# Performance work log

Measured on AMD Instinct MI355X. Metric: run time of the kernel, lower is better.

The kernel has to match this reference:

```python
import jax, jax.numpy as jnp
import numpy as np

NHEAD = 8
HEAD_DIM = 32  # per-head dim d; C = NHEAD * HEAD_DIM = 256
NEG_INF = -1e9


def setup_inputs() -> dict:
    key = jax.random.key(0)
    k1, k2, k3, k4, k5 = jax.random.split(key, 5)
    B, L, C = 8, 1024, NHEAD * HEAD_DIM
    query = jax.random.normal(k1, (B, L, C), dtype=jnp.float32)
    key_t = jax.random.normal(k2, (B, L, C), dtype=jnp.float32)
    value = jax.random.normal(k3, (B, L, C), dtype=jnp.float32)
    hard_mask = jax.random.randint(k4, (B, L), 0, 2).astype(bool)
    bias = jax.random.normal(k5, (B, L, L), dtype=jnp.float32)
    return {"query": query, "key": key_t, "value": value,
            "hard_mask": hard_mask, "bias": bias}


def reference(query, key, value, hard_mask, bias):
    # Faithful to the hard-mask path: attention is computed only among
    # active tokens (hard_mask True); inactive positions pass `value` through.
    # Masking inactive KEYS with -inf in the softmax is mathematically
    # identical to the sort/gather/slice/SDPA/scatter-unsort in the original.
    B, L, C = query.shape
    H, D = NHEAD, HEAD_DIM
    scale = 1.0 / jnp.sqrt(jnp.asarray(D, query.dtype))

    def split_heads(t):  # (B, L, C) -> (B, H, L, D)
        return t.reshape(B, L, H, D).transpose(0, 2, 1, 3)

    q, k, v = split_heads(query), split_heads(key), split_heads(value)

    # scores: (B, H, Lq, Lk); bias broadcasts over heads
    scores = jnp.einsum('bhld,bhmd->bhlm', q, k) * scale + bias[:, None, :, :]
    scores = jnp.where(hard_mask[:, None, None, :], scores, NEG_INF)
    attn = jax.nn.softmax(scores, axis=-1)
    out = jnp.einsum('bhlm,bhmd->bhld', attn, v)          # (B, H, L, D)
    out = out.transpose(0, 2, 1, 3).reshape(B, L, C)      # (B, L, C)

    # inactive query positions return the raw value (scatter-back behavior)
    out = jnp.where(hard_mask[:, :, None], out, value)

    # torch.stack over per-item (1, L, C) results -> (B, 1, L, C)
    return out[:, None, :, :]
```

## Files before the change

### kernel.cpp

```cpp
#include <hip/hip_runtime.h>
#include <hip/hip_bf16.h>

#define B_    8
#define H_    8
#define L_    1024
#define D_    32
#define C_    256
#define NK    64
#define PSTR  72

typedef __attribute__((ext_vector_type(8))) short bf16x8;
typedef __attribute__((ext_vector_type(4))) float f32x4;

__device__ inline unsigned short f2bf(float f) {
    union { float f; unsigned int u; } x; x.f = f;
    return (unsigned short)((x.u + 0x7fffu + ((x.u >> 16) & 1u)) >> 16);
}

__device__ inline unsigned int pk_bf16(float lo, float hi) {
    union { __hip_bfloat162 h; unsigned int u; } c;
    c.h = __float22bfloat162_rn(make_float2(lo, hi));
    return c.u;
}

__global__ __launch_bounds__(256) void prep_kv(
    const float* __restrict__ k, const float* __restrict__ v,
    unsigned short* __restrict__ kbf, unsigned short* __restrict__ vt)
{
    const int tid = threadIdx.x;
    const int blk = blockIdx.x;
    __shared__ float sTf[32][65];

    if (blk < 1024) {
        const size_t g = (size_t)blk * 2048 + (size_t)tid * 8;
        const int b   = (int)(g >> 18);
        const int r1  = (int)(g & 262143);
        const int key = r1 >> 8;
        const int h   = (r1 >> 5) & 7;
        const int d0  = r1 & 31;
        float4 f0 = ((const float4*)(k + g))[0];
        float4 f1 = ((const float4*)(k + g))[1];
        uint4 o;
        o.x = pk_bf16(f0.x, f0.y);
        o.y = pk_bf16(f0.z, f0.w);
        o.z = pk_bf16(f1.x, f1.y);
        o.w = pk_bf16(f1.z, f1.w);
        *(uint4*)(kbf + ((size_t)((b * 8 + h) * 1024 + key) * 32 + d0)) = o;
    } else {
        const int bid = blk - 1024;
        const int bh = bid >> 4, c = bid & 15;
        const int b = bh >> 3, h = bh & 7;
        {
            const int row = tid >> 2, d8 = (tid & 3) * 8;
            const float* src = v + ((size_t)(b * L_ + c * 64 + row) * C_ + h * D_ + d8);
            float4 a = ((const float4*)src)[0];
            float4 cc = ((const float4*)src)[1];
            sTf[d8 + 0][row] = a.x;  sTf[d8 + 1][row] = a.y;
            sTf[d8 + 2][row] = a.z;  sTf[d8 + 3][row] = a.w;
            sTf[d8 + 4][row] = cc.x; sTf[d8 + 5][row] = cc.y;
            sTf[d8 + 6][row] = cc.z; sTf[d8 + 7][row] = cc.w;
        }
        __syncthreads();
        {
            const int d = tid >> 3, seg = tid & 7;
            uint4 o;
            o.x = pk_bf16(sTf[d][seg * 8 + 0], sTf[d][seg * 8 + 1]);
            o.y = pk_bf16(sTf[d][seg * 8 + 2], sTf[d][seg * 8 + 3]);
            o.z = pk_bf16(sTf[d][seg * 8 + 4], sTf[d][seg * 8 + 5]);
            o.w = pk_bf16(sTf[d][seg * 8 + 6], sTf[d][seg * 8 + 7]);
            const int ap = seg ^ (d & 7);
            *(uint4*)(vt + ((size_t)((bh * 16 + c) * 32 + d) * 64 + ap * 8)) = o;
        }
    }
}

__global__ __launch_bounds__(256, 4) void attn_main(
    const float* __restrict__ q,
    const float* __restrict__ v,
    const int*   __restrict__ mask,
    const float* __restrict__ bias,
    const unsigned short* __restrict__ kbf,
    const unsigned short* __restrict__ vt,
    float*       __restrict__ out)
{
    __shared__ __align__(16) unsigned short sK[2][NK * D_];
    __shared__ __align__(16) unsigned short sV[2][D_ * NK];
    __shared__ float sMadd[L_];
    __shared__ __align__(16) unsigned short sP[4][16][PSTR];

    const int tid  = threadIdx.x;
    const int wv   = tid >> 6;
    const int ln   = tid & 63;
    const int l16  = ln & 15;
    const int quad = ln >> 4;

    const int blk = blockIdx.x;
    const int h   = blk >> 7;
    const int rem = blk & 127;
    const int b   = rem >> 4;
    const int qt  = rem & 15;
    const int q0  = qt * 64 + wv * 16;
    const int bh  = b * H_ + h;

    const float scale = 0.17677669529663687f;

    {
        int4 m = ((const int4*)(mask + b * L_))[tid];
        sMadd[tid * 4 + 0] = m.x ? 0.f : -1e9f;
        sMadd[tid * 4 + 1] = m.y ? 0.f : -1e9f;
        sMadd[tid * 4 + 2] = m.z ? 0.f : -1e9f;
        sMadd[tid * 4 + 3] = m.w ? 0.f : -1e9f;
    }

    bf16x8 qfrag;
    {
        const float* qp = q + ((size_t)(b * L_ + q0 + l16) * C_ + h * D_ + quad * 8);
        float4 a = ((const float4*)qp)[0];
        float4 c = ((const float4*)qp)[1];
        __align__(16) unsigned int u[4] = {
            pk_bf16(a.x, a.y), pk_bf16(a.z, a.w),
            pk_bf16(c.x, c.y), pk_bf16(c.z, c.w)};
        qfrag = *(const bf16x8*)u;
    }

    const unsigned short* kt  = kbf + (size_t)bh * L_ * D_;
    const unsigned short* vtb = vt  + (size_t)bh * 16 * D_ * NK;

    uint4 kreg = *(const uint4*)(kt  + tid * 8);
    uint4 vreg = *(const uint4*)(vtb + tid * 8);
    *(uint4*)(&sK[0][tid * 8]) = kreg;
    *(uint4*)(&sV[0][tid * 8]) = vreg;
    __syncthreads();

    f32x4 Oacc[2] = {{0.f,0.f,0.f,0.f},{0.f,0.f,0.f,0.f}};
    float psum[4] = {0.f, 0.f, 0.f, 0.f};
    const size_t brow0 = (size_t)(b * L_ + q0 + quad * 4) * L_;

    for (int c = 0; c < 16; ++c) {
        const int cur = c & 1;
        const int j0  = c * NK;

        if (c < 15) {
            kreg = *(const uint4*)(kt  + (c + 1) * 2048 + tid * 8);
            vreg = *(const uint4*)(vtb + (c + 1) * 2048 + tid * 8);
        }

        float bz[4][4];
#pragma unroll
        for (int nt = 0; nt < 4; ++nt)
#pragma unroll
            for (int r = 0; r < 4; ++r)
                bz[nt][r] = bias[brow0 + (size_t)r * L_ + j0 + nt * 16 + l16];

        bf16x8 kf[4];
#pragma unroll
        for (int nt = 0; nt < 4; ++nt)
            kf[nt] = *(const bf16x8*)&sK[cur][(nt * 16 + l16) * D_ + quad * 8];

        f32x4 S[4];
#pragma unroll
        for (int nt = 0; nt < 4; ++nt)
            S[nt] = __builtin_amdgcn_mfma_f32_16x16x32_bf16(
                qfrag, kf[nt], (f32x4){0.f,0.f,0.f,0.f}, 0, 0, 0);

        float madd[4];
#pragma unroll
        for (int nt = 0; nt < 4; ++nt)
            madd[nt] = sMadd[j0 + nt * 16 + l16];

#pragma unroll
        for (int nt = 0; nt < 4; ++nt) {
#pragma unroll
            for (int r = 0; r < 4; ++r) {
                float t = bz[nt][r] + madd[nt];
                float p = __expf(fmaf(S[nt][r], scale, t));
                psum[r] += p;
                S[nt][r] = p;
            }
        }

#pragma unroll
        for (int nt = 0; nt < 4; ++nt) {
#pragma unroll
            for (int r = 0; r < 4; r += 2) {
                unsigned int u = pk_bf16(S[nt][r], S[nt][r + 1]);
                sP[wv][quad * 4 + r    ][nt * 16 + l16] = (unsigned short)u;
                sP[wv][quad * 4 + r + 1][nt * 16 + l16] = (unsigned short)(u >> 16);
            }
        }

#pragma unroll
        for (int s2 = 0; s2 < 2; ++s2) {
            bf16x8 pf = *(const bf16x8*)&sP[wv][l16][s2 * 32 + quad * 8];
#pragma unroll
            for (int nt = 0; nt < 2; ++nt) {
                const int d  = nt * 16 + l16;
                const int ap = (s2 * 4 + quad) ^ (l16 & 7);
                bf16x8 vf = *(const bf16x8*)&sV[cur][d * NK + ap * 8];
                Oacc[nt] = __builtin_amdgcn_mfma_f32_16x16x32_bf16(pf, vf, Oacc[nt], 0, 0, 0);
            }
        }

        if (c < 15) {
            *(uint4*)(&sK[cur ^ 1][tid * 8]) = kreg;
            *(uint4*)(&sV[cur ^ 1][tid * 8]) = vreg;
            __syncthreads();
        }
    }

#pragma unroll
    for (int r = 0; r < 4; ++r) {
        float t = psum[r];
        t += __shfl_xor(t, 1);
        t += __shfl_xor(t, 2);
        t += __shfl_xor(t, 4);
        t += __shfl_xor(t, 8);
        const int qrow = q0 + quad * 4 + r;
        const float inv = 1.f / t;
        const bool active = (sMadd[qrow] == 0.f);
        const size_t base = (size_t)(b * L_ + qrow) * C_ + h * D_;
#pragma unroll
        for (int nt = 0; nt < 2; ++nt) {
            const size_t idx = base + nt * 16 + l16;
            out[idx] = active ? Oacc[nt][r] * inv : v[idx];
        }
    }
}

#define MQ    64
#define KSTR  48
#define VSTR  72

__global__ __launch_bounds__(256) void masked_attn_mfma(
    const float* __restrict__ q,
    const float* __restrict__ k,
    const float* __restrict__ v,
    const int*   __restrict__ mask,
    const float* __restrict__ bias,
    float*       __restrict__ out)
{
    __shared__ __align__(16) unsigned short sQ[MQ][KSTR];
    __shared__ __align__(16) unsigned short sKt[NK][KSTR];
    __shared__ __align__(16) unsigned short sVt[D_][VSTR];
    __shared__ __align__(16) unsigned short sP2[4][16][VSTR];
    __shared__ float sMadd2[NK];

    const int tid  = threadIdx.x;
    const int wv   = tid >> 6;
    const int ln   = tid & 63;
    const int l16  = ln & 15;
    const int quad = ln >> 4;

    const int blk = blockIdx.x;
    const int h   = blk & 7;
    const int qt  = (blk >> 3) & 15;
    const int b   = blk >> 7;
    const int q0  = qt * MQ;
    const float scale = 0.17677669529663687f;

    {
        const int row = tid >> 2, d0 = (tid & 3) * 8;
        const float* src = q + ((size_t)(b * L_ + q0 + row) * C_ + h * D_ + d0);
        float4 a = ((const float4*)src)[0];
        float4 c = ((const float4*)src)[1];
        __align__(16) unsigned short t8[8] = {
            f2bf(a.x), f2bf(a.y), f2bf(a.z), f2bf(a.w),
            f2bf(c.x), f2bf(c.y), f2bf(c.z), f2bf(c.w)};
        *(int4*)&sQ[row][d0] = *(const int4*)t8;
    }
    __syncthreads();

    const bf16x8 qfrag = *(const bf16x8*)&sQ[wv * 16 + l16][quad * 8];
    f32x4 Oacc[2] = {{0.f,0.f,0.f,0.f},{0.f,0.f,0.f,0.f}};
    float lsum[4] = {0.f, 0.f, 0.f, 0.f};

    for (int j0 = 0; j0 < L_; j0 += NK) {
        __syncthreads();
        {
            const int row = tid >> 2, d0 = (tid & 3) * 8;
            const size_t src = (size_t)(b * L_ + j0 + row) * C_ + h * D_ + d0;
            float4 ka = ((const float4*)(k + src))[0];
            float4 kb = ((const float4*)(k + src))[1];
            __align__(16) unsigned short t8[8] = {
                f2bf(ka.x), f2bf(ka.y), f2bf(ka.z), f2bf(ka.w),
                f2bf(kb.x), f2bf(kb.y), f2bf(kb.z), f2bf(kb.w)};
            *(int4*)&sKt[row][d0] = *(const int4*)t8;

            float4 va = ((const float4*)(v + src))[0];
            float4 vb = ((const float4*)(v + src))[1];
            sVt[d0 + 0][row] = f2bf(va.x);
            sVt[d0 + 1][row] = f2bf(va.y);
            sVt[d0 + 2][row] = f2bf(va.z);
            sVt[d0 + 3][row] = f2bf(va.w);
            sVt[d0 + 4][row] = f2bf(vb.x);
            sVt[d0 + 5][row] = f2bf(vb.y);
            sVt[d0 + 6][row] = f2bf(vb.z);
            sVt[d0 + 7][row] = f2bf(vb.w);
            if (tid < NK) sMadd2[tid] = mask[b * L_ + j0 + tid] ? 0.f : -1e9f;
        }
        __syncthreads();

        bf16x8 kf[4];
#pragma unroll
        for (int nt = 0; nt < 4; ++nt)
            kf[nt] = *(const bf16x8*)&sKt[nt * 16 + l16][quad * 8];

        f32x4 S[4];
#pragma unroll
        for (int nt = 0; nt < 4; ++nt)
            S[nt] = __builtin_amdgcn_mfma_f32_16x16x32_bf16(
                qfrag, kf[nt], (f32x4){0.f,0.f,0.f,0.f}, 0, 0, 0);

        float psum[4] = {0.f, 0.f, 0.f, 0.f};
        const size_t brow0 = (size_t)(b * L_ + q0 + wv * 16 + quad * 4) * L_ + j0;
#pragma unroll
        for (int nt = 0; nt < 4; ++nt) {
            const float madd = sMadd2[nt * 16 + l16];
#pragma unroll
            for (int r = 0; r < 4; ++r) {
                float s = S[nt][r] * scale + bias[brow0 + (size_t)r * L_ + nt * 16 + l16] + madd;
                float p = __expf(s);
                psum[r] += p;
                S[nt][r] = p;
            }
        }
#pragma unroll
        for (int nt = 0; nt < 4; ++nt)
#pragma unroll
            for (int r = 0; r < 4; ++r)
                sP2[wv][quad * 4 + r][nt * 16 + l16] = f2bf(S[nt][r]);
#pragma unroll
        for (int r = 0; r < 4; ++r) {
            float t = psum[r];
            t += __shfl_xor(t, 1);
            t += __shfl_xor(t, 2);
            t += __shfl_xor(t, 4);
            t += __shfl_xor(t, 8);
            lsum[r] += t;
        }
#pragma unroll
        for (int s2 = 0; s2 < 2; ++s2) {
            bf16x8 pf = *(const bf16x8*)&sP2[wv][l16][s2 * 32 + quad * 8];
#pragma unroll
            for (int nt = 0; nt < 2; ++nt) {
                bf16x8 vf = *(const bf16x8*)&sVt[nt * 16 + l16][s2 * 32 + quad * 8];
                Oacc[nt] = __builtin_amdgcn_mfma_f32_16x16x32_bf16(pf, vf, Oacc[nt], 0, 0, 0);
            }
        }
    }
#pragma unroll
    for (int r = 0; r < 4; ++r) {
        const int qg = q0 + wv * 16 + quad * 4 + r;
        const int active = mask[b * L_ + qg];
        const size_t obase = (size_t)(b * L_ + qg) * C_ + h * D_;
        const float inv = 1.f / lsum[r];
#pragma unroll
        for (int nt = 0; nt < 2; ++nt) {
            float val;
            if (active) val = Oacc[nt][r] * inv;
            else        val = v[obase + nt * 16 + l16];
            out[obase + nt * 16 + l16] = val;
        }
    }
}

extern "C" void kernel_launch(void* const* d_in, const int* in_sizes, int n_in,
                              void* d_out, int out_size, void* d_ws, size_t ws_size,
                              hipStream_t stream) {
    const float* q    = (const float*)d_in[0];
    const float* k    = (const float*)d_in[1];
    const float* v    = (const float*)d_in[2];
    const int*   mask = (const int*)d_in[3];
    const float* bias = (const float*)d_in[4];
    float* out = (float*)d_out;

    if (ws_size >= (size_t)8 * 1024 * 1024) {
        unsigned short* kbf = (unsigned short*)d_ws;
        unsigned short* vt  = kbf + (size_t)2 * 1024 * 1024;
        prep_kv<<<2048, 256, 0, stream>>>(k, v, kbf, vt);
        attn_main<<<1024, 256, 0, stream>>>(q, v, mask, bias, kbf, vt, out);
    } else {
        masked_attn_mfma<<<1024, 256, 0, stream>>>(q, k, v, mask, bias, out);
    }
}
```

Baseline: 124.8 us.

## Pre-pack K/V into MFMA fragment layout and drop LDS staging in attention loop

The prep kernel now writes K and V as bf16 in the exact per-lane MFMA fragment order, so the main kernel loads fragments straight from global memory without shared-memory double buffering or per-chunk barriers. Scores pass through LDS in fp32, so bias is read row-contiguous as float4 and added together with the mask after the transpose. Scale is folded into Q, and the row sums are computed by an extra MFMA against a ones vector instead of a shuffle reduction. The cost is per-wave global fragment loads with no cross-wave reuse and no explicit prefetch, plus one more MFMA per sub-tile.

```diff
diff --git a/kernel.cpp b/kernel.cpp
--- a/kernel.cpp
+++ b/kernel.cpp
@@ -7,7 +7,6 @@
 #define D_    32
 #define C_    256
 #define NK    64
-#define PSTR  72
 
 typedef __attribute__((ext_vector_type(8))) short bf16x8;
 typedef __attribute__((ext_vector_type(4))) float f32x4;
@@ -23,70 +22,67 @@
     return c.u;
 }
 
-__global__ __launch_bounds__(256) void prep_kv(
+__global__ __launch_bounds__(256) void prep_frag(
     const float* __restrict__ k, const float* __restrict__ v,
-    unsigned short* __restrict__ kbf, unsigned short* __restrict__ vt)
+    unsigned short* __restrict__ kfrag, unsigned short* __restrict__ vfrag)
 {
     const int tid = threadIdx.x;
     const int blk = blockIdx.x;
-    __shared__ float sTf[32][65];
-
-    if (blk < 1024) {
-        const size_t g = (size_t)blk * 2048 + (size_t)tid * 8;
-        const int b   = (int)(g >> 18);
-        const int r1  = (int)(g & 262143);
-        const int key = r1 >> 8;
-        const int h   = (r1 >> 5) & 7;
-        const int d0  = r1 & 31;
-        float4 f0 = ((const float4*)(k + g))[0];
-        float4 f1 = ((const float4*)(k + g))[1];
-        uint4 o;
-        o.x = pk_bf16(f0.x, f0.y);
-        o.y = pk_bf16(f0.z, f0.w);
-        o.z = pk_bf16(f1.x, f1.y);
-        o.w = pk_bf16(f1.z, f1.w);
-        *(uint4*)(kbf + ((size_t)((b * 8 + h) * 1024 + key) * 32 + d0)) = o;
-    } else {
-        const int bid = blk - 1024;
-        const int bh = bid >> 4, c = bid & 15;
-        const int b = bh >> 3, h = bh & 7;
-        {
-            const int row = tid >> 2, d8 = (tid & 3) * 8;
-            const float* src = v + ((size_t)(b * L_ + c * 64 + row) * C_ + h * D_ + d8);
-            float4 a = ((const float4*)src)[0];
-            float4 cc = ((const float4*)src)[1];
-            sTf[d8 + 0][row] = a.x;  sTf[d8 + 1][row] = a.y;
-            sTf[d8 + 2][row] = a.z;  sTf[d8 + 3][row] = a.w;
-            sTf[d8 + 4][row] = cc.x; sTf[d8 + 5][row] = cc.y;
-            sTf[d8 + 6][row] = cc.z; sTf[d8 + 7][row] = cc.w;
-        }
-        __syncthreads();
-        {
-            const int d = tid >> 3, seg = tid & 7;
-            uint4 o;
-            o.x = pk_bf16(sTf[d][seg * 8 + 0], sTf[d][seg * 8 + 1]);
-            o.y = pk_bf16(sTf[d][seg * 8 + 2], sTf[d][seg * 8 + 3]);
-            o.z = pk_bf16(sTf[d][seg * 8 + 4], sTf[d][seg * 8 + 5]);
-            o.w = pk_bf16(sTf[d][seg * 8 + 6], sTf[d][seg * 8 + 7]);
-            const int ap = seg ^ (d & 7);
-            *(uint4*)(vt + ((size_t)((bh * 16 + c) * 32 + d) * 64 + ap * 8)) = o;
-        }
-    }
-}
-
-__global__ __launch_bounds__(256, 4) void attn_main(
+    const int bh = blk >> 4, c = blk & 15;
+    const int b = bh >> 3, h = bh & 7;
+
+    __shared__ float sKf[64 * 36];
+    __shared__ float sVf[64 * 33];
+
+    {
+        const int row = tid >> 2, seg = tid & 3;
+        const size_t src = (size_t)(b * L_ + c * 64 + row) * C_ + h * D_ + seg * 8;
+        float4 a = *(const float4*)(k + src);
+        float4 d = *(const float4*)(k + src + 4);
+        *(float4*)(sKf + row * 36 + seg * 8) = a;
+        *(float4*)(sKf + row * 36 + seg * 8 + 4) = d;
+        float4 va = *(const float4*)(v + src);
+        float4 vd = *(const float4*)(v + src + 4);
+        float* vr = sVf + row * 33 + seg * 8;
+        vr[0] = va.x; vr[1] = va.y; vr[2] = va.z; vr[3] = va.w;
+        vr[4] = vd.x; vr[5] = vd.y; vr[6] = vd.z; vr[7] = vd.w;
+    }
+    __syncthreads();
+
+    const int ln = tid & 63, u = tid >> 6;
+    const int l16 = ln & 15, quad = ln >> 4;
+
+    {
+        const float* src = sKf + (u * 16 + l16) * 36 + quad * 8;
+        float4 a = *(const float4*)src;
+        float4 d = *(const float4*)(src + 4);
+        uint4 o = { pk_bf16(a.x, a.y), pk_bf16(a.z, a.w),
+                    pk_bf16(d.x, d.y), pk_bf16(d.z, d.w) };
+        *(uint4*)(kfrag + (size_t)blk * 2048 + u * 512 + ln * 8) = o;
+    }
+    {
+        const int s2 = u >> 1, nt = u & 1;
+        float vals[8];
+#pragma unroll
+        for (int j = 0; j < 8; ++j)
+            vals[j] = sVf[(s2 * 32 + quad * 8 + j) * 33 + nt * 16 + l16];
+        uint4 o = { pk_bf16(vals[0], vals[1]), pk_bf16(vals[2], vals[3]),
+                    pk_bf16(vals[4], vals[5]), pk_bf16(vals[6], vals[7]) };
+        *(uint4*)(vfrag + (size_t)blk * 2048 + s2 * 1024 + nt * 512 + ln * 8) = o;
+    }
+}
+
+__global__ __launch_bounds__(256, 4) void attn_fa(
     const float* __restrict__ q,
     const float* __restrict__ v,
     const int*   __restrict__ mask,
     const float* __restrict__ bias,
-    const unsigned short* __restrict__ kbf,
-    const unsigned short* __restrict__ vt,
+    const unsigned short* __restrict__ kfrag,
+    const unsigned short* __restrict__ vfrag,
     float*       __restrict__ out)
 {
-    __shared__ __align__(16) unsigned short sK[2][NK * D_];
-    __shared__ __align__(16) unsigned short sV[2][D_ * NK];
     __shared__ float sMadd[L_];
-    __shared__ __align__(16) unsigned short sP[4][16][PSTR];
+    __shared__ float sS[4][16 * 68];
 
     const int tid  = threadIdx.x;
     const int wv   = tid >> 6;
@@ -111,6 +107,7 @@
         sMadd[tid * 4 + 2] = m.z ? 0.f : -1e9f;
         sMadd[tid * 4 + 3] = m.w ? 0.f : -1e9f;
     }
+    __syncthreads();
 
     bf16x8 qfrag;
     {
@@ -118,105 +115,87 @@
         float4 a = ((const float4*)qp)[0];
         float4 c = ((const float4*)qp)[1];
         __align__(16) unsigned int u[4] = {
-            pk_bf16(a.x, a.y), pk_bf16(a.z, a.w),
-            pk_bf16(c.x, c.y), pk_bf16(c.z, c.w)};
+            pk_bf16(a.x * scale, a.y * scale), pk_bf16(a.z * scale, a.w * scale),
+            pk_bf16(c.x * scale, c.y * scale), pk_bf16(c.z * scale, c.w * scale)};
         qfrag = *(const bf16x8*)u;
     }
 
-    const unsigned short* kt  = kbf + (size_t)bh * L_ * D_;
-    const unsigned short* vtb = vt  + (size_t)bh * 16 * D_ * NK;
-
-    uint4 kreg = *(const uint4*)(kt  + tid * 8);
-    uint4 vreg = *(const uint4*)(vtb + tid * 8);
-    *(uint4*)(&sK[0][tid * 8]) = kreg;
-    *(uint4*)(&sV[0][tid * 8]) = vreg;
-    __syncthreads();
+    bf16x8 onesf;
+#pragma unroll
+    for (int i = 0; i < 8; ++i) onesf[i] = (short)0x3F80;
+
+    const unsigned short* kf_base = kfrag + (size_t)bh * 32768 + ln * 8;
+    const unsigned short* vf_base = vfrag + (size_t)bh * 32768 + ln * 8;
+    const float* bias_row = bias + (size_t)(b * L_ + q0 + l16) * L_;
+    float* const sSw   = &sS[wv][0];
+    const float* sSrow = &sS[wv][0] + l16 * 68;
 
     f32x4 Oacc[2] = {{0.f,0.f,0.f,0.f},{0.f,0.f,0.f,0.f}};
-    float psum[4] = {0.f, 0.f, 0.f, 0.f};
-    const size_t brow0 = (size_t)(b * L_ + q0 + quad * 4) * L_;
+    f32x4 Lacc    = {0.f,0.f,0.f,0.f};
 
     for (int c = 0; c < 16; ++c) {
-        const int cur = c & 1;
-        const int j0  = c * NK;
-
-        if (c < 15) {
-            kreg = *(const uint4*)(kt  + (c + 1) * 2048 + tid * 8);
-            vreg = *(const uint4*)(vtb + (c + 1) * 2048 + tid * 8);
-        }
-
-        float bz[4][4];
+        const int j0 = c * NK;
+
+        const unsigned short* kp = kf_base + c * 2048;
+        bf16x8 kf0 = *(const bf16x8*)(kp);
+        bf16x8 kf1 = *(const bf16x8*)(kp + 512);
+        bf16x8 kf2 = *(const bf16x8*)(kp + 1024);
+        bf16x8 kf3 = *(const bf16x8*)(kp + 1536);
+
+        f32x4 S[4];
+        S[0] = __builtin_amdgcn_mfma_f32_16x16x32_bf16(qfrag, kf0, (f32x4){0.f,0.f,0.f,0.f}, 0, 0, 0);
+        S[1] = __builtin_amdgcn_mfma_f32_16x16x32_bf16(qfrag, kf1, (f32x4){0.f,0.f,0.f,0.f}, 0, 0, 0);
+        S[2] = __builtin_amdgcn_mfma_f32_16x16x32_bf16(qfrag, kf2, (f32x4){0.f,0.f,0.f,0.f}, 0, 0, 0);
+        S[3] = __builtin_amdgcn_mfma_f32_16x16x32_bf16(qfrag, kf3, (f32x4){0.f,0.f,0.f,0.f}, 0, 0, 0);
+
 #pragma unroll
         for (int nt = 0; nt < 4; ++nt)
 #pragma unroll
             for (int r = 0; r < 4; ++r)
-                bz[nt][r] = bias[brow0 + (size_t)r * L_ + j0 + nt * 16 + l16];
-
-        bf16x8 kf[4];
-#pragma unroll
-        for (int nt = 0; nt < 4; ++nt)
-            kf[nt] = *(const bf16x8*)&sK[cur][(nt * 16 + l16) * D_ + quad * 8];
-
-        f32x4 S[4];
-#pragma unroll
-        for (int nt = 0; nt < 4; ++nt)
-            S[nt] = __builtin_amdgcn_mfma_f32_16x16x32_bf16(
-                qfrag, kf[nt], (f32x4){0.f,0.f,0.f,0.f}, 0, 0, 0);
-
-        float madd[4];
-#pragma unroll
-        for (int nt = 0; nt < 4; ++nt)
-            madd[nt] = sMadd[j0 + nt * 16 + l16];
-
-#pragma unroll
-        for (int nt = 0; nt < 4; ++nt) {
-#pragma unroll
-            for (int r = 0; r < 4; ++r) {
-                float t = bz[nt][r] + madd[nt];
-                float p = __expf(fmaf(S[nt][r], scale, t));
-                psum[r] += p;
-                S[nt][r] = p;
+                sSw[(quad * 4 + r) * 68 + nt * 16 + l16] = S[nt][r];
+
+        bf16x8 pf[2];
+#pragma unroll
+        for (int s2 = 0; s2 < 2; ++s2) {
+            const float* sr = sSrow + s2 * 32 + quad * 8;
+            float4 a0 = *(const float4*)(sr);
+            float4 a1 = *(const float4*)(sr + 4);
+            const float* bp = bias_row + j0 + s2 * 32 + quad * 8;
+            float4 b0 = *(const float4*)(bp);
+            float4 b1 = *(const float4*)(bp + 4);
+            const float* mp = sMadd + j0 + s2 * 32 + quad * 8;
+            float4 m0 = *(const float4*)(mp);
+            float4 m1 = *(const float4*)(mp + 4);
+            float p0 = __expf(a0.x + b0.x + m0.x);
+            float p1 = __expf(a0.y + b0.y + m0.y);
+            float p2 = __expf(a0.z + b0.z + m0.z);
+            float p3 = __expf(a0.w + b0.w + m0.w);
+            float p4 = __expf(a1.x + b1.x + m1.x);
+            float p5 = __expf(a1.y + b1.y + m1.y);
+            float p6 = __expf(a1.z + b1.z + m1.z);
+            float p7 = __expf(a1.w + b1.w + m1.w);
+            __align__(16) unsigned int u[4] = {
+                pk_bf16(p0, p1), pk_bf16(p2, p3),
+                pk_bf16(p4, p5), pk_bf16(p6, p7)};
+            pf[s2] = *(const bf16x8*)u;
+        }
+
+        const unsigned short* vp = vf_base + c * 2048;
+#pragma unroll
+        for (int s2 = 0; s2 < 2; ++s2) {
+            Lacc = __builtin_amdgcn_mfma_f32_16x16x32_bf16(pf[s2], onesf, Lacc, 0, 0, 0);
+#pragma unroll
+            for (int nt = 0; nt < 2; ++nt) {
+                bf16x8 vfr = *(const bf16x8*)(vp + s2 * 1024 + nt * 512);
+                Oacc[nt] = __builtin_amdgcn_mfma_f32_16x16x32_bf16(pf[s2], vfr, Oacc[nt], 0, 0, 0);
             }
         }
-
-#pragma unroll
-        for (int nt = 0; nt < 4; ++nt) {
-#pragma unroll
-            for (int r = 0; r < 4; r += 2) {
-                unsigned int u = pk_bf16(S[nt][r], S[nt][r + 1]);
-                sP[wv][quad * 4 + r    ][nt * 16 + l16] = (unsigned short)u;
-                sP[wv][quad * 4 + r + 1][nt * 16 + l16] = (unsigned short)(u >> 16);
-            }
-        }
-
-#pragma unroll
-        for (int s2 = 0; s2 < 2; ++s2) {
-            bf16x8 pf = *(const bf16x8*)&sP[wv][l16][s2 * 32 + quad * 8];
-#pragma unroll
-            for (int nt = 0; nt < 2; ++nt) {
-                const int d  = nt * 16 + l16;
-                const int ap = (s2 * 4 + quad) ^ (l16 & 7);
-                bf16x8 vf = *(const bf16x8*)&sV[cur][d * NK + ap * 8];
-                Oacc[nt] = __builtin_amdgcn_mfma_f32_16x16x32_bf16(pf, vf, Oacc[nt], 0, 0, 0);
-            }
-        }
-
-        if (c < 15) {
-            *(uint4*)(&sK[cur ^ 1][tid * 8]) = kreg;
-            *(uint4*)(&sV[cur ^ 1][tid * 8]) = vreg;
-            __syncthreads();
-        }
     }
 
 #pragma unroll
     for (int r = 0; r < 4; ++r) {
-        float t = psum[r];
-        t += __shfl_xor(t, 1);
-        t += __shfl_xor(t, 2);
-        t += __shfl_xor(t, 4);
-        t += __shfl_xor(t, 8);
         const int qrow = q0 + quad * 4 + r;
-        const float inv = 1.f / t;
+        const float inv = 1.f / Lacc[r];
         const bool active = (sMadd[qrow] == 0.f);
         const size_t base = (size_t)(b * L_ + qrow) * C_ + h * D_;
 #pragma unroll
@@ -375,10 +354,10 @@
     float* out = (float*)d_out;
 
     if (ws_size >= (size_t)8 * 1024 * 1024) {
-        unsigned short* kbf = (unsigned short*)d_ws;
-        unsigned short* vt  = kbf + (size_t)2 * 1024 * 1024;
-        prep_kv<<<2048, 256, 0, stream>>>(k, v, kbf, vt);
-        attn_main<<<1024, 256, 0, stream>>>(q, v, mask, bias, kbf, vt, out);
+        unsigned short* kfrag = (unsigned short*)d_ws;
+        unsigned short* vfrag = kfrag + (size_t)2 * 1024 * 1024;
+        prep_frag<<<1024, 256, 0, stream>>>(k, v, kfrag, vfrag);
+        attn_fa<<<1024, 256, 0, stream>>>(q, v, mask, bias, kfrag, vfrag, out);
     } else {
         masked_attn_mfma<<<1024, 256, 0, stream>>>(q, k, v, mask, bias, out);
     }
```

Result: slower. 144.3 us (+15.6%).
